# Optimization experiments

Measured on AMD Instinct MI355X. Metric: run time of the kernel, lower is better.

The kernel has to match this reference:

```python
import jax, jax.numpy as jnp
import numpy as np

H, W = 512, 512
N_GAUSS = 4096
T_EPS = 1e-3          # early-termination threshold from the torch loop
COV_DIAG = 25.0       # hardcoded cov_2d = eye(2) * 25 in rasterize_gaussians


def quat_to_rot(q):
    # standard (w, x, y, z) quaternion -> rotation matrix, with normalization
    q = q / jnp.linalg.norm(q)
    w, x, y, z = q[0], q[1], q[2], q[3]
    return jnp.array([
        [1 - 2 * (y * y + z * z), 2 * (x * y - w * z),     2 * (x * z + w * y)],
        [2 * (x * y + w * z),     1 - 2 * (x * x + z * z), 2 * (y * z - w * x)],
        [2 * (x * z - w * y),     2 * (y * z + w * x),     1 - 2 * (x * x + y * y)],
    ])


def setup_inputs() -> dict:
    key = jax.random.key(0)
    k0, k1, k2, k3 = jax.random.split(key, 4)
    xy = jax.random.uniform(k0, (N_GAUSS, 2), minval=-2.0, maxval=2.0)
    z = jax.random.uniform(k1, (N_GAUSS, 1), minval=4.0, maxval=10.0)
    positions = jnp.concatenate([xy, z], axis=-1)                    # [N,3], z>0
    colors = jax.random.uniform(k2, (N_GAUSS, 3))                    # [N,3] in [0,1]
    opacities = jax.random.uniform(k3, (N_GAUSS,)) * 0.5             # [N]
    quaternion = jnp.array([1.0, 0.05, 0.02, 0.01], dtype=jnp.float32)
    cam_position = jnp.zeros(3, dtype=jnp.float32)
    intrinsics = jnp.array([[500.0, 0.0, 256.0],
                            [0.0, 500.0, 256.0],
                            [0.0, 0.0, 1.0]], dtype=jnp.float32)
    background_color = jnp.zeros(3, dtype=jnp.float32)
    return {"positions": positions, "colors": colors, "opacities": opacities,
            "quaternion": quaternion, "cam_position": cam_position,
            "intrinsics": intrinsics, "background_color": background_color}


def _render(positions, colors, opacities, quaternion, cam_position, intrinsics,
            background_color):
    R = quat_to_rot(quaternion)                                      # [3,3]
    pos_cam = (positions - cam_position[None, :]) @ R.T              # [N,3]
    proj = pos_cam @ intrinsics.T                                    # [N,3]
    screen = proj[:, :2] / proj[:, 2:3]                              # [N,2]
    depths = proj[:, 2]                                              # [N]

    order = jnp.argsort(-depths)                                     # back-to-front
    centers_s = screen[order]
    colors_s = colors[order]
    opac_s = opacities[order]
    depth_s = pos_cam[order, 2]

    yy, xx = jnp.meshgrid(jnp.arange(H, dtype=jnp.float32),
                          jnp.arange(W, dtype=jnp.float32), indexing="ij")
    pix = jnp.stack([xx, yy], axis=-1)                               # [H,W,2] (x,y)

    init_color = jnp.broadcast_to(background_color[:, None, None], (3, H, W))
    carry0 = (init_color, jnp.zeros((H, W)), jnp.zeros((H, W)), jnp.ones((H, W)))

    def step(carry, g):
        color_acc, depth_acc, alpha_acc, T = carry
        center, color, opacity, depth = g
        # emulate the `if transmittance.max() < 1e-3: break` exactly: once T
        # saturates it is monotone, so masking all later contributions == break
        active = (jnp.max(T) >= T_EPS).astype(T.dtype)
        diff = pix - center[None, None, :]                           # [H,W,2]
        mahal = jnp.sum(diff * diff, axis=-1) / COV_DIAG             # cov_inv = I/25
        alpha = jnp.clip(jnp.exp(-0.5 * mahal) * opacity, 0.0, 1.0) * active
        ta = T * alpha
        color_acc = color_acc + ta[None, :, :] * color[:, None, None]
        depth_acc = depth_acc + ta * depth
        alpha_acc = alpha_acc + ta
        T = T * (1.0 - alpha)
        return (color_acc, depth_acc, alpha_acc, T), None

    (image, depth_map, alpha_map, _), _ = jax.lax.scan(
        step, carry0, (centers_s, colors_s, opac_s, depth_s))
    return image, depth_map, alpha_map


def reference(positions, colors, opacities, quaternion, cam_position, intrinsics,
              background_color):
    return _render(positions, colors, opacities, quaternion, cam_position,
                   intrinsics, background_color)
```

## Files before the change

### kernel.cpp

```cpp
#include <hip/hip_runtime.h>
#include <hip/hip_bf16.h>

#define N_GAUSS 4096
#define H 512
#define W 512
#define HW (H * W)
#define SEG 4
#define CULL2 1444.0f
#define MAXS 1024


__global__ __launch_bounds__(256) void prep_kernel(
        const float* __restrict__ pos, const float* __restrict__ colors,
        const float* __restrict__ opac, const float* __restrict__ quat,
        const float* __restrict__ cam, const float* __restrict__ Km,
        float4* __restrict__ pxyz, float4* __restrict__ pcol) {
    int i = blockIdx.x * 256 + threadIdx.x;
    float qw = quat[0], qx = quat[1], qy = quat[2], qz = quat[3];
    float qn = 1.0f / sqrtf(qw * qw + qx * qx + qy * qy + qz * qz);
    qw *= qn; qx *= qn; qy *= qn; qz *= qn;
    float r00 = 1.f - 2.f * (qy * qy + qz * qz), r01 = 2.f * (qx * qy - qw * qz), r02 = 2.f * (qx * qz + qw * qy);
    float r10 = 2.f * (qx * qy + qw * qz), r11 = 1.f - 2.f * (qx * qx + qz * qz), r12 = 2.f * (qy * qz - qw * qx);
    float r20 = 2.f * (qx * qz - qw * qy), r21 = 2.f * (qy * qz + qw * qx), r22 = 1.f - 2.f * (qx * qx + qy * qy);
    float ax = pos[3 * i] - cam[0], ay = pos[3 * i + 1] - cam[1], az = pos[3 * i + 2] - cam[2];
    float X = r00 * ax + r01 * ay + r02 * az;
    float Y = r10 * ax + r11 * ay + r12 * az;
    float Z = r20 * ax + r21 * ay + r22 * az;
    float u = Km[0] * X + Km[1] * Y + Km[2] * Z;
    float v = Km[3] * X + Km[4] * Y + Km[5] * Z;
    float w = Km[6] * X + Km[7] * Y + Km[8] * Z;
    pxyz[i] = make_float4(u / w, v / w, Z, opac[i]);
    pcol[i] = make_float4(colors[3 * i], colors[3 * i + 1], colors[3 * i + 2], 0.f);
}

__global__ __launch_bounds__(1024, 8) void render_all_kernel(
        const float4* __restrict__ pxyz, const float4* __restrict__ pcol,
        const float* __restrict__ bg, float* __restrict__ out) {
    __shared__ __align__(16) float skey[MAXS + 4];
    __shared__ __align__(16) unsigned short sidxs[MAXS + 4];
    __shared__ __align__(16) float4 srec[MAXS];
    __shared__ __align__(16) float4 scol[MAXS];
    __shared__ float comb[SEG][6][256];
    __shared__ int scnt;

    int tid = threadIdx.x;
    int lane = tid & 63;
    int wave = tid >> 6;
    int seg = wave >> 2;
    int p = tid & 255;
    int tile = (blockIdx.x * 341) & 1023;
    int tx0 = (tile & 31) * 16, ty0 = (tile >> 5) * 16;
    float px = (float)(tx0 + (p & 15)), py = (float)(ty0 + (p >> 4));
    float tcx = tx0 + 7.5f, tcy = ty0 + 7.5f;

    if (tid == 0) scnt = 0;
    __syncthreads();

    #pragma unroll
    for (int k = 0; k < 4; ++k) {
        int g = k * 1024 + tid;
        float4 P = pxyz[g];
        float ddx = P.x - tcx, ddy = P.y - tcy;
        bool pred = (ddx * ddx + ddy * ddy <= CULL2);
        unsigned long long m = __ballot(pred ? 1 : 0);
        int base = 0;
        if (lane == 0) base = atomicAdd(&scnt, __popcll(m));
        base = __shfl(base, 0);
        if (pred) {
            int slot = base + __popcll(m & ((1ull << lane) - 1ull));
            if (slot < MAXS) {
                skey[slot] = P.z;
                sidxs[slot] = (unsigned short)g;
                srec[slot] = P;
            }
        }
    }
    __syncthreads();
    int n = min(scnt, MAXS);
    if (tid < 4) { skey[n + tid] = -1e30f; sidxs[n + tid] = 0; }
    __syncthreads();

    float4 rec;
    int r = 0;
    if (tid < n) {
        float Zi = skey[tid];
        int idxi = sidxs[tid];
        rec = srec[tid];
        int pad4 = (n + 3) & ~3;
        for (int j = 0; j < pad4; j += 4) {
            float4 kz = *reinterpret_cast<const float4*>(&skey[j]);
            ushort4 si = *reinterpret_cast<const ushort4*>(&sidxs[j]);
            r += (kz.x > Zi) || (kz.x == Zi && (int)si.x < idxi);
            r += (kz.y > Zi) || (kz.y == Zi && (int)si.y < idxi);
            r += (kz.z > Zi) || (kz.z == Zi && (int)si.z < idxi);
            r += (kz.w > Zi) || (kz.w == Zi && (int)si.w < idxi);
        }
    }
    __syncthreads();
    if (tid < n) {
        srec[r] = rec;
        scol[r] = pcol[sidxs[tid]];
    }
    __syncthreads();

    int q = (n + 3) >> 2;
    int beg = min(seg * q, n), end = min(beg + q, n);
    float T = 1.f, cr = 0.f, cg = 0.f, cb = 0.f, da = 0.f, aa = 0.f;
    #pragma unroll 2
    for (int g = beg; g < end; ++g) {
        float4 GA = srec[g];
        float dx = px - GA.x, dy = py - GA.y;
        float al = __expf(-0.02f * (dx * dx + dy * dy)) * GA.w;
        float ta = T * al;
        float4 GC = scol[g];
        cr += ta * GC.x; cg += ta * GC.y; cb += ta * GC.z;
        da += ta * GA.z; aa += ta;
        T -= ta;
    }

    comb[seg][0][p] = cr;  comb[seg][1][p] = cg;  comb[seg][2][p] = cb;
    comb[seg][3][p] = da;  comb[seg][4][p] = aa;  comb[seg][5][p] = T;
    __syncthreads();
    if (seg == 0) {
        float r2 = 0.f, g2 = 0.f, b2 = 0.f, d2 = 0.f, a2 = 0.f;
        #pragma unroll
        for (int s = SEG - 1; s >= 0; --s) {
            float Ts = comb[s][5][p];
            r2 = comb[s][0][p] + Ts * r2;
            g2 = comb[s][1][p] + Ts * g2;
            b2 = comb[s][2][p] + Ts * b2;
            d2 = comb[s][3][p] + Ts * d2;
            a2 = comb[s][4][p] + Ts * a2;
        }
        int pid = (ty0 + (p >> 4)) * W + tx0 + (p & 15);
        out[pid]          = bg[0] + r2;
        out[HW + pid]     = bg[1] + g2;
        out[2 * HW + pid] = bg[2] + b2;
        out[3 * HW + pid] = d2;
        out[4 * HW + pid] = a2;
    }
}

extern "C" void kernel_launch(void* const* d_in, const int* in_sizes, int n_in,
                              void* d_out, int out_size, void* d_ws, size_t ws_size,
                              hipStream_t stream) {
    const float* positions = (const float*)d_in[0];
    const float* colors    = (const float*)d_in[1];
    const float* opacities = (const float*)d_in[2];
    const float* quat      = (const float*)d_in[3];
    const float* cam       = (const float*)d_in[4];
    const float* intr      = (const float*)d_in[5];
    const float* bg        = (const float*)d_in[6];
    float* out = (float*)d_out;

    float4* pxyz = (float4*)d_ws;
    float4* pcol = (float4*)((char*)d_ws + 65536);

    prep_kernel<<<dim3(16), dim3(256), 0, stream>>>(
        positions, colors, opacities, quat, cam, intr, pxyz, pcol);
    render_all_kernel<<<dim3(1024), dim3(1024), 0, stream>>>(
        pxyz, pcol, bg, out);
}
```

Measured before the change: 105.1 us.

## Use persistent blocks with atomic tile queue and packed 64-bit sort keys

The render kernel now launches a fixed number of persistent blocks that pull tiles from a global atomic counter, which prep_kernel initializes. The goal is to balance the uneven per-tile cost and cut block launch overhead. The rank sort also packs depth bits and the inverted Gaussian index into a single 64-bit key, so each comparison is one integer compare instead of a float compare plus a tie-break. Costs are a serial atomic and barrier between tiles, heavier 64-bit shared-memory traffic, and dropping the occupancy hint from launch_bounds.

```diff
diff --git a/kernel.cpp b/kernel.cpp
--- a/kernel.cpp
+++ b/kernel.cpp
@@ -8,14 +8,17 @@
 #define SEG 4
 #define CULL2 1444.0f
 #define MAXS 1024
+#define NBLOCKS 512
 
 
 __global__ __launch_bounds__(256) void prep_kernel(
         const float* __restrict__ pos, const float* __restrict__ colors,
         const float* __restrict__ opac, const float* __restrict__ quat,
         const float* __restrict__ cam, const float* __restrict__ Km,
-        float4* __restrict__ pxyz, float4* __restrict__ pcol) {
+        float4* __restrict__ pxyz, float4* __restrict__ pcol,
+        int* __restrict__ counter) {
     int i = blockIdx.x * 256 + threadIdx.x;
+    if (i == 0) *counter = NBLOCKS;
     float qw = quat[0], qx = quat[1], qy = quat[2], qz = quat[3];
     float qn = 1.0f / sqrtf(qw * qw + qx * qx + qy * qy + qz * qz);
     qw *= qn; qx *= qn; qy *= qn; qz *= qn;
@@ -33,111 +36,119 @@
     pcol[i] = make_float4(colors[3 * i], colors[3 * i + 1], colors[3 * i + 2], 0.f);
 }
 
-__global__ __launch_bounds__(1024, 8) void render_all_kernel(
+__global__ __launch_bounds__(1024) void render_all_kernel(
         const float4* __restrict__ pxyz, const float4* __restrict__ pcol,
-        const float* __restrict__ bg, float* __restrict__ out) {
-    __shared__ __align__(16) float skey[MAXS + 4];
-    __shared__ __align__(16) unsigned short sidxs[MAXS + 4];
+        const float* __restrict__ bg, float* __restrict__ out,
+        int* __restrict__ counter) {
+    __shared__ __align__(16) unsigned long long skey[MAXS + 4];
     __shared__ __align__(16) float4 srec[MAXS];
     __shared__ __align__(16) float4 scol[MAXS];
     __shared__ float comb[SEG][6][256];
     __shared__ int scnt;
+    __shared__ int snext;
 
     int tid = threadIdx.x;
     int lane = tid & 63;
-    int wave = tid >> 6;
-    int seg = wave >> 2;
+    int seg = tid >> 8;
     int p = tid & 255;
-    int tile = (blockIdx.x * 341) & 1023;
-    int tx0 = (tile & 31) * 16, ty0 = (tile >> 5) * 16;
-    float px = (float)(tx0 + (p & 15)), py = (float)(ty0 + (p >> 4));
-    float tcx = tx0 + 7.5f, tcy = ty0 + 7.5f;
 
-    if (tid == 0) scnt = 0;
-    __syncthreads();
+    int tile = blockIdx.x;
+    while (tile < 1024) {
+        int swz = (tile * 341) & 1023;
+        int tx0 = (swz & 31) * 16, ty0 = (swz >> 5) * 16;
+        float px = (float)(tx0 + (p & 15)), py = (float)(ty0 + (p >> 4));
+        float tcx = tx0 + 7.5f, tcy = ty0 + 7.5f;
 
-    #pragma unroll
-    for (int k = 0; k < 4; ++k) {
-        int g = k * 1024 + tid;
-        float4 P = pxyz[g];
-        float ddx = P.x - tcx, ddy = P.y - tcy;
-        bool pred = (ddx * ddx + ddy * ddy <= CULL2);
-        unsigned long long m = __ballot(pred ? 1 : 0);
-        int base = 0;
-        if (lane == 0) base = atomicAdd(&scnt, __popcll(m));
-        base = __shfl(base, 0);
-        if (pred) {
-            int slot = base + __popcll(m & ((1ull << lane) - 1ull));
-            if (slot < MAXS) {
-                skey[slot] = P.z;
-                sidxs[slot] = (unsigned short)g;
-                srec[slot] = P;
+        if (tid == 0) scnt = 0;
+        __syncthreads();
+
+        #pragma unroll
+        for (int k = 0; k < 4; ++k) {
+            int g = k * 1024 + tid;
+            float4 P = pxyz[g];
+            float ddx = P.x - tcx, ddy = P.y - tcy;
+            bool pred = (ddx * ddx + ddy * ddy <= CULL2);
+            unsigned long long m = __ballot(pred ? 1 : 0);
+            int base = 0;
+            if (lane == 0) base = atomicAdd(&scnt, __popcll(m));
+            base = __shfl(base, 0);
+            if (pred) {
+                int slot = base + __popcll(m & ((1ull << lane) - 1ull));
+                if (slot < MAXS) {
+                    skey[slot] = ((unsigned long long)__float_as_uint(P.z) << 12)
+                               | (unsigned)(4095 - g);
+                    srec[slot] = P;
+                }
             }
         }
-    }
-    __syncthreads();
-    int n = min(scnt, MAXS);
-    if (tid < 4) { skey[n + tid] = -1e30f; sidxs[n + tid] = 0; }
-    __syncthreads();
+        __syncthreads();
+        int n = min(scnt, MAXS);
+        if (tid < 4) skey[n + tid] = 0ull;
+        __syncthreads();
 
-    float4 rec;
-    int r = 0;
-    if (tid < n) {
-        float Zi = skey[tid];
-        int idxi = sidxs[tid];
-        rec = srec[tid];
-        int pad4 = (n + 3) & ~3;
-        for (int j = 0; j < pad4; j += 4) {
-            float4 kz = *reinterpret_cast<const float4*>(&skey[j]);
-            ushort4 si = *reinterpret_cast<const ushort4*>(&sidxs[j]);
-            r += (kz.x > Zi) || (kz.x == Zi && (int)si.x < idxi);
-            r += (kz.y > Zi) || (kz.y == Zi && (int)si.y < idxi);
-            r += (kz.z > Zi) || (kz.z == Zi && (int)si.z < idxi);
-            r += (kz.w > Zi) || (kz.w == Zi && (int)si.w < idxi);
+        float4 rec;
+        int r = 0, gidx = 0;
+        if (tid < n) {
+            unsigned long long ki = skey[tid];
+            gidx = 4095 - (int)(ki & 0xFFFull);
+            rec = srec[tid];
+            int pad4 = (n + 3) & ~3;
+            for (int j = 0; j < pad4; j += 4) {
+                ulonglong2 a = *reinterpret_cast<const ulonglong2*>(&skey[j]);
+                ulonglong2 b = *reinterpret_cast<const ulonglong2*>(&skey[j + 2]);
+                r += (a.x > ki);
+                r += (a.y > ki);
+                r += (b.x > ki);
+                r += (b.y > ki);
+            }
         }
-    }
-    __syncthreads();
-    if (tid < n) {
-        srec[r] = rec;
-        scol[r] = pcol[sidxs[tid]];
-    }
-    __syncthreads();
+        __syncthreads();
+        if (tid < n) {
+            srec[r] = rec;
+            scol[r] = pcol[gidx];
+        }
+        __syncthreads();
 
-    int q = (n + 3) >> 2;
-    int beg = min(seg * q, n), end = min(beg + q, n);
-    float T = 1.f, cr = 0.f, cg = 0.f, cb = 0.f, da = 0.f, aa = 0.f;
-    #pragma unroll 2
-    for (int g = beg; g < end; ++g) {
-        float4 GA = srec[g];
-        float dx = px - GA.x, dy = py - GA.y;
-        float al = __expf(-0.02f * (dx * dx + dy * dy)) * GA.w;
-        float ta = T * al;
-        float4 GC = scol[g];
-        cr += ta * GC.x; cg += ta * GC.y; cb += ta * GC.z;
-        da += ta * GA.z; aa += ta;
-        T -= ta;
-    }
+        int q = (n + 3) >> 2;
+        int beg = min(seg * q, n), end = min(beg + q, n);
+        float T = 1.f, cr = 0.f, cg = 0.f, cb = 0.f, da = 0.f, aa = 0.f;
+        #pragma unroll 2
+        for (int g = beg; g < end; ++g) {
+            float4 GA = srec[g];
+            float dx = px - GA.x, dy = py - GA.y;
+            float al = __expf(-0.02f * (dx * dx + dy * dy)) * GA.w;
+            float ta = T * al;
+            float4 GC = scol[g];
+            cr += ta * GC.x; cg += ta * GC.y; cb += ta * GC.z;
+            da += ta * GA.z; aa += ta;
+            T -= ta;
+        }
 
-    comb[seg][0][p] = cr;  comb[seg][1][p] = cg;  comb[seg][2][p] = cb;
-    comb[seg][3][p] = da;  comb[seg][4][p] = aa;  comb[seg][5][p] = T;
-    __syncthreads();
-    if (seg == 0) {
-        float r2 = 0.f, g2 = 0.f, b2 = 0.f, d2 = 0.f, a2 = 0.f;
-        #pragma unroll
-        for (int s = SEG - 1; s >= 0; --s) {
-            float Ts = comb[s][5][p];
-            r2 = comb[s][0][p] + Ts * r2;
-            g2 = comb[s][1][p] + Ts * g2;
-            b2 = comb[s][2][p] + Ts * b2;
-            d2 = comb[s][3][p] + Ts * d2;
-            a2 = comb[s][4][p] + Ts * a2;
+        comb[seg][0][p] = cr;  comb[seg][1][p] = cg;  comb[seg][2][p] = cb;
+        comb[seg][3][p] = da;  comb[seg][4][p] = aa;  comb[seg][5][p] = T;
+        __syncthreads();
+        if (seg == 0) {
+            float r2 = 0.f, g2 = 0.f, b2 = 0.f, d2 = 0.f, a2 = 0.f;
+            #pragma unroll
+            for (int s = SEG - 1; s >= 0; --s) {
+                float Ts = comb[s][5][p];
+                r2 = comb[s][0][p] + Ts * r2;
+                g2 = comb[s][1][p] + Ts * g2;
+                b2 = comb[s][2][p] + Ts * b2;
+                d2 = comb[s][3][p] + Ts * d2;
+                a2 = comb[s][4][p] + Ts * a2;
+            }
+            int pid = (ty0 + (p >> 4)) * W + tx0 + (p & 15);
+            out[pid]          = bg[0] + r2;
+            out[HW + pid]     = bg[1] + g2;
+            out[2 * HW + pid] = bg[2] + b2;
+            out[3 * HW + pid] = d2;
+            out[4 * HW + pid] = a2;
         }
-        int pid = (ty0 + (p >> 4)) * W + tx0 + (p & 15);
-        out[pid]          = bg[0] + r2;
-        out[HW + pid]     = bg[1] + g2;
-        out[2 * HW + pid] = bg[2] + b2;
-        out[3 * HW + pid] = d2;
-        out[4 * HW + pid] = a2;
+
+        if (tid == 0) snext = atomicAdd(counter, 1);
+        __syncthreads();
+        tile = snext;
     }
 }
 
@@ -155,9 +166,10 @@
 
     float4* pxyz = (float4*)d_ws;
     float4* pcol = (float4*)((char*)d_ws + 65536);
+    int* counter = (int*)((char*)d_ws + 131072);
 
     prep_kernel<<<dim3(16), dim3(256), 0, stream>>>(
-        positions, colors, opacities, quat, cam, intr, pxyz, pcol);
-    render_all_kernel<<<dim3(1024), dim3(1024), 0, stream>>>(
-        pxyz, pcol, bg, out);
+        positions, colors, opacities, quat, cam, intr, pxyz, pcol, counter);
+    render_all_kernel<<<dim3(NBLOCKS), dim3(1024), 0, stream>>>(
+        pxyz, pcol, bg, out, counter);
 }
```

Result: faster. 102.4 us (-2.6%).

## Use 256-thread tiles with a single compositing segment and packed 64-bit sort keys

Applied to the files above, without the earlier changes.

Replaces the 1024-thread block, which split the depth-sorted gaussian list into four segments and recombined them through shared memory, with a 256-thread block that walks the whole list per pixel. The depth and index pair is packed into one 64-bit key so the rank sort needs a single unsigned comparison, with each thread ranking two entries. MAXS drops to 512, which cuts shared memory per block. In exchange, each thread's serial compositing loop becomes longer, and tiles with more than 512 culled gaussians would be silently truncated.

```diff
diff --git a/kernel.cpp b/kernel.cpp
--- a/kernel.cpp
+++ b/kernel.cpp
@@ -5,9 +5,8 @@
 #define H 512
 #define W 512
 #define HW (H * W)
-#define SEG 4
 #define CULL2 1444.0f
-#define MAXS 1024
+#define MAXS 512
 
 
 __global__ __launch_bounds__(256) void prep_kernel(
@@ -33,32 +32,27 @@
     pcol[i] = make_float4(colors[3 * i], colors[3 * i + 1], colors[3 * i + 2], 0.f);
 }
 
-__global__ __launch_bounds__(1024, 8) void render_all_kernel(
+__global__ __launch_bounds__(256) void render_tile_kernel(
         const float4* __restrict__ pxyz, const float4* __restrict__ pcol,
         const float* __restrict__ bg, float* __restrict__ out) {
-    __shared__ __align__(16) float skey[MAXS + 4];
-    __shared__ __align__(16) unsigned short sidxs[MAXS + 4];
+    __shared__ __align__(16) unsigned long long skey[MAXS + 4];
     __shared__ __align__(16) float4 srec[MAXS];
     __shared__ __align__(16) float4 scol[MAXS];
-    __shared__ float comb[SEG][6][256];
     __shared__ int scnt;
 
     int tid = threadIdx.x;
     int lane = tid & 63;
-    int wave = tid >> 6;
-    int seg = wave >> 2;
-    int p = tid & 255;
-    int tile = (blockIdx.x * 341) & 1023;
+    int tile = blockIdx.x;
     int tx0 = (tile & 31) * 16, ty0 = (tile >> 5) * 16;
-    float px = (float)(tx0 + (p & 15)), py = (float)(ty0 + (p >> 4));
+    float px = (float)(tx0 + (tid & 15)), py = (float)(ty0 + (tid >> 4));
     float tcx = tx0 + 7.5f, tcy = ty0 + 7.5f;
 
     if (tid == 0) scnt = 0;
     __syncthreads();
 
-    #pragma unroll
-    for (int k = 0; k < 4; ++k) {
-        int g = k * 1024 + tid;
+    #pragma unroll 4
+    for (int k = 0; k < 16; ++k) {
+        int g = k * 256 + tid;
         float4 P = pxyz[g];
         float ddx = P.x - tcx, ddy = P.y - tcy;
         bool pred = (ddx * ddx + ddy * ddy <= CULL2);
@@ -69,45 +63,38 @@
         if (pred) {
             int slot = base + __popcll(m & ((1ull << lane) - 1ull));
             if (slot < MAXS) {
-                skey[slot] = P.z;
-                sidxs[slot] = (unsigned short)g;
+                skey[slot] = ((unsigned long long)__float_as_uint(P.z) << 12)
+                           | (unsigned)(4095 - g);
                 srec[slot] = P;
             }
         }
     }
     __syncthreads();
     int n = min(scnt, MAXS);
-    if (tid < 4) { skey[n + tid] = -1e30f; sidxs[n + tid] = 0; }
+    if (tid < 4) skey[n + tid] = 0ull;
     __syncthreads();
 
-    float4 rec;
-    int r = 0;
-    if (tid < n) {
-        float Zi = skey[tid];
-        int idxi = sidxs[tid];
-        rec = srec[tid];
-        int pad4 = (n + 3) & ~3;
-        for (int j = 0; j < pad4; j += 4) {
-            float4 kz = *reinterpret_cast<const float4*>(&skey[j]);
-            ushort4 si = *reinterpret_cast<const ushort4*>(&sidxs[j]);
-            r += (kz.x > Zi) || (kz.x == Zi && (int)si.x < idxi);
-            r += (kz.y > Zi) || (kz.y == Zi && (int)si.y < idxi);
-            r += (kz.z > Zi) || (kz.z == Zi && (int)si.z < idxi);
-            r += (kz.w > Zi) || (kz.w == Zi && (int)si.w < idxi);
-        }
+    bool a0 = (tid < n), a1 = (tid + 256 < n);
+    unsigned long long k0 = 0, k1 = 0;
+    float4 rec0, rec1;
+    int g0 = 0, g1 = 0, r0 = 0, r1 = 0;
+    if (a0) { k0 = skey[tid];       rec0 = srec[tid];       g0 = 4095 - (int)(k0 & 0xFFFull); }
+    if (a1) { k1 = skey[tid + 256]; rec1 = srec[tid + 256]; g1 = 4095 - (int)(k1 & 0xFFFull); }
+    int pad4 = (n + 3) & ~3;
+    for (int j = 0; j < pad4; j += 4) {
+        ulonglong2 a = *reinterpret_cast<const ulonglong2*>(&skey[j]);
+        ulonglong2 b = *reinterpret_cast<const ulonglong2*>(&skey[j + 2]);
+        r0 += (a.x > k0) + (a.y > k0) + (b.x > k0) + (b.y > k0);
+        r1 += (a.x > k1) + (a.y > k1) + (b.x > k1) + (b.y > k1);
     }
     __syncthreads();
-    if (tid < n) {
-        srec[r] = rec;
-        scol[r] = pcol[sidxs[tid]];
-    }
+    if (a0) { srec[r0] = rec0; scol[r0] = pcol[g0]; }
+    if (a1) { srec[r1] = rec1; scol[r1] = pcol[g1]; }
     __syncthreads();
 
-    int q = (n + 3) >> 2;
-    int beg = min(seg * q, n), end = min(beg + q, n);
-    float T = 1.f, cr = 0.f, cg = 0.f, cb = 0.f, da = 0.f, aa = 0.f;
+    float T = 1.f, cr = bg[0], cg = bg[1], cb = bg[2], da = 0.f, aa = 0.f;
     #pragma unroll 2
-    for (int g = beg; g < end; ++g) {
+    for (int g = 0; g < n; ++g) {
         float4 GA = srec[g];
         float dx = px - GA.x, dy = py - GA.y;
         float al = __expf(-0.02f * (dx * dx + dy * dy)) * GA.w;
@@ -118,27 +105,12 @@
         T -= ta;
     }
 
-    comb[seg][0][p] = cr;  comb[seg][1][p] = cg;  comb[seg][2][p] = cb;
-    comb[seg][3][p] = da;  comb[seg][4][p] = aa;  comb[seg][5][p] = T;
-    __syncthreads();
-    if (seg == 0) {
-        float r2 = 0.f, g2 = 0.f, b2 = 0.f, d2 = 0.f, a2 = 0.f;
-        #pragma unroll
-        for (int s = SEG - 1; s >= 0; --s) {
-            float Ts = comb[s][5][p];
-            r2 = comb[s][0][p] + Ts * r2;
-            g2 = comb[s][1][p] + Ts * g2;
-            b2 = comb[s][2][p] + Ts * b2;
-            d2 = comb[s][3][p] + Ts * d2;
-            a2 = comb[s][4][p] + Ts * a2;
-        }
-        int pid = (ty0 + (p >> 4)) * W + tx0 + (p & 15);
-        out[pid]          = bg[0] + r2;
-        out[HW + pid]     = bg[1] + g2;
-        out[2 * HW + pid] = bg[2] + b2;
-        out[3 * HW + pid] = d2;
-        out[4 * HW + pid] = a2;
-    }
+    int pid = (ty0 + (tid >> 4)) * W + tx0 + (tid & 15);
+    out[pid]          = cr;
+    out[HW + pid]     = cg;
+    out[2 * HW + pid] = cb;
+    out[3 * HW + pid] = da;
+    out[4 * HW + pid] = aa;
 }
 
 extern "C" void kernel_launch(void* const* d_in, const int* in_sizes, int n_in,
@@ -158,6 +130,6 @@
 
     prep_kernel<<<dim3(16), dim3(256), 0, stream>>>(
         positions, colors, opacities, quat, cam, intr, pxyz, pcol);
-    render_all_kernel<<<dim3(1024), dim3(1024), 0, stream>>>(
+    render_tile_kernel<<<dim3(1024), dim3(256), 0, stream>>>(
         pxyz, pcol, bg, out);
 }
```

Result: faster. 98.14 us (-6.7%).
